# Optimization experiments

Measured on AMD Instinct MI355X. Metric: run time of the kernel, lower is better.

## Reference

```python
import jax, jax.numpy as jnp
import numpy as np


def setup_inputs() -> dict:
    key = jax.random.key(0)
    k1, k2 = jax.random.split(key)
    x = jax.random.normal(k1, (16, 1024, 512), dtype=jnp.float32)
    embedding = jax.random.normal(k2, (8192, 512), dtype=jnp.float32)
    return {"x": x, "embedding": embedding}


def reference(x, embedding):
    # x: [b, n, c], embedding (codebook k): [m, c]
    b, n, c = x.shape
    m = embedding.shape[0]
    q = x.reshape(b * n, c)            # (b n) c
    k = embedding
    # Squared L2 distance: ||q||^2 + ||k||^2 - 2 q.k  -> [bn, m]
    sim = (jnp.sum(q * q, axis=1, keepdims=True)
           + jnp.sum(k * k, axis=1)
           - 2.0 * jnp.einsum('nc,mc->nm', q, k))
    z_indices = jnp.argmin(sim, axis=1)                     # [bn]
    z_onehot = jax.nn.one_hot(z_indices, m, dtype=jnp.float32)  # [bn, m]
    # Direct gather is mathematically identical to onehot @ k
    z = k[z_indices]                                        # [bn, c]
    # Straight-through estimator: z = q + sg(z - q)
    z_st = q + jax.lax.stop_gradient(z - q)
    # Perplexity of code usage
    z_mean = jnp.mean(z_onehot, axis=0)                     # [m]
    perplexity = jnp.exp(-jnp.sum(z_mean * jnp.log(z_mean + 1e-10)))
    return (z_st.reshape(b, n, c),
            z_indices.reshape(b, n),
            z_onehot.reshape(b, n, m),
            perplexity)
```

## Files before the change

kernel.cpp:

```cpp
#include <hip/hip_runtime.h>
#include <cstdint>
#include <cstddef>

#define BNR 16384
#define C   512
#define M   8192
#define BM  128
#define BN  128
#define BK  64
#define NCH 8
#define NSETS 64

#define GEMM_BLOCKS 8192
#define NZ1 256
#define R1  8192
#define NZ2 128
#define R2  10240
#define FIN_FULL 1536
#define FIN_SCAT 40

#define TILE_U16   8192
#define PANEL_U16  65536

typedef float f32x4 __attribute__((ext_vector_type(4)));
typedef _Float16 f16x8 __attribute__((ext_vector_type(8)));
typedef unsigned short u16;

static __device__ __forceinline__ u16 h_bits(_Float16 h) {
    union { _Float16 h; u16 u; } x; x.h = h; return x.u;
}
static __device__ __forceinline__ void gl_lds16(const void* g, void* l) {
    __builtin_amdgcn_global_load_lds(
        (const __attribute__((address_space(1))) void*)g,
        (__attribute__((address_space(3))) void*)l, 16, 0, 0);
}

static __device__ __forceinline__ void cvt_unit(const float* __restrict__ in,
                                                u16* __restrict__ outp, int o) {
    int q = o & 1023, kb = q >> 7, row = q & 127;
    int c = (o >> 10) & 7, pan = o >> 13;
    int grow = pan * BM + row;
    int k0 = c * BK + kb * 8;
    const float4* src = (const float4*)(in + (size_t)grow * C + k0);
    float4 a = src[0], b = src[1];
    u16 v[8] = { h_bits((_Float16)a.x), h_bits((_Float16)a.y),
                 h_bits((_Float16)a.z), h_bits((_Float16)a.w),
                 h_bits((_Float16)b.x), h_bits((_Float16)b.y),
                 h_bits((_Float16)b.z), h_bits((_Float16)b.w) };
    u16* dst = outp + (size_t)o * 8;
    *(ushort4*)(dst)     = *(ushort4*)(v);
    *(ushort4*)(dst + 4) = *(ushort4*)(v + 4);
}

__global__ void prelude_k(const float* __restrict__ x, const float* __restrict__ emb,
                          u16* __restrict__ x2t, u16* __restrict__ e2t,
                          float* __restrict__ knorm) {
    int b = blockIdx.x;
    if (b < 4096) { cvt_unit(x, x2t, b * 256 + threadIdx.x); return; }
    if (b < 6144) { cvt_unit(emb, e2t, (b - 4096) * 256 + threadIdx.x); return; }
    int t = (b - 6144) * 256 + threadIdx.x;
    int gw = t >> 6, lane = t & 63;
    for (int row = gw; row < M; row += 256) {
        const float4* p = (const float4*)(emb + (size_t)row * C);
        float s = 0.f;
#pragma unroll
        for (int j = 0; j < 2; ++j) {
            float4 v = p[lane + 64 * j];
            s += v.x * v.x + v.y * v.y + v.z * v.z + v.w * v.w;
        }
#pragma unroll
        for (int o = 32; o > 0; o >>= 1) s += __shfl_down(s, o, 64);
        if (lane == 0) knorm[row] = s;
    }
}

__global__ void mega_k(
    const u16* __restrict__ x2t, const u16* __restrict__ e2t,
    const float* __restrict__ knorm,
    float* __restrict__ pv1, int* __restrict__ pi1,
    float* __restrict__ pv2, int* __restrict__ pi2,
    float* __restrict__ onehot) {
    __shared__ __align__(16) u16 ldsA[8][128][8];
    __shared__ __align__(16) u16 ldsB[8][128][8];

    if (blockIdx.x < NZ1) {
        f32x4* o4 = (f32x4*)onehot;
        size_t base = (size_t)blockIdx.x * 65536 + threadIdx.x;
        const f32x4 z = (f32x4)(0.0f);
#pragma unroll 4
        for (int i = 0; i < 256; ++i)
            __builtin_nontemporal_store(z, &o4[base + (size_t)i * 256]);
        return;
    }

    const int gid  = blockIdx.x - NZ1;
    const int tid  = threadIdx.x;
    const int lane = tid & 63;
    const int w    = tid >> 6;
    const int wm   = w >> 1, wn = w & 1;
    const int g    = lane >> 4, r = lane & 15;

    const int xk = gid & 7, j = gid >> 3;
    const int stid = (j >> 6) * 8 + xk;
    const int p  = j & 63;
    const int rb = (stid & 15) * 8 + (p & 7);
    const int cb = (stid >> 4) * 8 + (p >> 3);
    const int rowBase = rb * BM, colBase = cb * BN;

    f32x4 acc[4][4];
#pragma unroll
    for (int m = 0; m < 4; ++m)
#pragma unroll
        for (int n = 0; n < 4; ++n) acc[m][n] = (f32x4)(0.0f);

    const u16* aT = x2t + (size_t)rb * PANEL_U16;
    const u16* bT = e2t + (size_t)cb * PANEL_U16;

#pragma unroll 1
    for (int c = 0; c < NCH; ++c) {
        if (c) __syncthreads();
#pragma unroll
        for (int it = 0; it < 4; ++it) {
            int u = it * 256 + tid;
            gl_lds16(aT + (size_t)c * TILE_U16 + u * 8, (u16*)ldsA + u * 8);
            gl_lds16(bT + (size_t)c * TILE_U16 + u * 8, (u16*)ldsB + u * 8);
        }
        __syncthreads();

#pragma unroll
        for (int ks = 0; ks < 2; ++ks) {
            const int kb = ks * 4 + g;
            f16x8 a[4], b[4];
#pragma unroll
            for (int m = 0; m < 4; ++m)
                a[m] = *(const f16x8*)&ldsA[kb][wm * 64 + m * 16 + r][0];
#pragma unroll
            for (int n = 0; n < 4; ++n)
                b[n] = *(const f16x8*)&ldsB[kb][wn * 64 + n * 16 + r][0];
#pragma unroll
            for (int m = 0; m < 4; ++m)
#pragma unroll
                for (int n = 0; n < 4; ++n)
                    acc[m][n] = __builtin_amdgcn_mfma_f32_16x16x32_f16(
                        a[m], b[n], acc[m][n], 0, 0, 0);
        }
    }
    __syncthreads();

    float kn[4];
#pragma unroll
    for (int n = 0; n < 4; ++n) kn[n] = knorm[colBase + wn * 64 + n * 16 + r];

    float* mv = (float*)&ldsA[0][0][0];
    int*   mi = (int*)(mv + 2 * 128 * 2);

#pragma unroll
    for (int m = 0; m < 4; ++m) {
#pragma unroll
        for (int q = 0; q < 4; ++q) {
            float v1 = 3.0e38f, v2 = 3.0e38f;
            int   i1 = 0x7fffffff, i2 = 0x7fffffff;
#pragma unroll
            for (int n = 0; n < 4; ++n) {
                int col = colBase + wn * 64 + n * 16 + r;
                float d = fmaf(-2.0f, acc[m][n][q], kn[n]);
                if (d < v1 || (d == v1 && col < i1)) {
                    v2 = v1; i2 = i1; v1 = d; i1 = col;
                } else if (d < v2 || (d == v2 && col < i2)) {
                    v2 = d; i2 = col;
                }
            }
#pragma unroll
            for (int msk = 1; msk < 16; msk <<= 1) {
                float ov1 = __shfl_xor(v1, msk, 64);
                int   oi1 = __shfl_xor(i1, msk, 64);
                float ov2 = __shfl_xor(v2, msk, 64);
                int   oi2 = __shfl_xor(i2, msk, 64);
                bool ob = (ov1 < v1) || (ov1 == v1 && oi1 < i1);
                float nbv = ob ? ov1 : v1;  int nbi = ob ? oi1 : i1;
                float c1v = ob ? ov2 : v2;  int c1i = ob ? oi2 : i2;
                float c2v = ob ? v1 : ov1;  int c2i = ob ? i1 : oi1;
                bool cb2 = (c2v < c1v) || (c2v == c1v && c2i < c1i);
                v1 = nbv; i1 = nbi;
                v2 = cb2 ? c2v : c1v; i2 = cb2 ? c2i : c1i;
            }
            if (r == 0) {
                int lrow = wm * 64 + m * 16 + g * 4 + q;
                mv[(wn * 128 + lrow) * 2 + 0] = v1;
                mv[(wn * 128 + lrow) * 2 + 1] = v2;
                mi[(wn * 128 + lrow) * 2 + 0] = i1;
                mi[(wn * 128 + lrow) * 2 + 1] = i2;
            }
        }
    }
    __syncthreads();

    if (tid < 128) {
        float V1 = 3.0e38f, V2 = 3.0e38f;
        int   I1 = 0x7fffffff, I2 = 0x7fffffff;
#pragma unroll
        for (int s = 0; s < 4; ++s) {
            float d = mv[((s >> 1) * 128 + tid) * 2 + (s & 1)];
            int   ci = mi[((s >> 1) * 128 + tid) * 2 + (s & 1)];
            if (d < V1 || (d == V1 && ci < I1)) {
                V2 = V1; I2 = I1; V1 = d; I1 = ci;
            } else if (d < V2 || (d == V2 && ci < I2)) {
                V2 = d; I2 = ci;
            }
        }
        size_t o = (size_t)cb * BNR + rowBase + tid;
        pv1[o] = V1; pi1[o] = I1;
        pv2[o] = V2; pi2[o] = I2;
    }
}

__global__ void refine2_k(const float* __restrict__ x, const float* __restrict__ emb,
                          const float* __restrict__ pv1, const int* __restrict__ pi1,
                          const float* __restrict__ pv2, const int* __restrict__ pi2,
                          float* __restrict__ out_idx, float* __restrict__ zst,
                          float* __restrict__ onehot) {
    if (blockIdx.x < NZ2) {
        f32x4* o4 = (f32x4*)onehot;
        size_t base = (size_t)R1 * 2048 + (size_t)blockIdx.x * 32768 + threadIdx.x;
        const f32x4 z = (f32x4)(0.0f);
#pragma unroll 4
        for (int i = 0; i < 128; ++i)
            __builtin_nontemporal_store(z, &o4[base + (size_t)i * 256]);
        return;
    }
    int rid  = blockIdx.x - NZ2;
    int row  = rid * 4 + (threadIdx.x >> 6);
    int lane = threadIdx.x & 63;
    size_t off = (size_t)lane * BNR + row;
    float va = pv1[off]; int ia = pi1[off];
    float vb = pv2[off]; int ib = pi2[off];
    int cand[8];
#pragma unroll
    for (int b = 0; b < 8; ++b) {
        bool al = (va < vb) || (va == vb && ia < ib);
        float cv = al ? va : vb; int ci = al ? ia : ib;
#pragma unroll
        for (int msk = 1; msk < 64; msk <<= 1) {
            float ov = __shfl_xor(cv, msk, 64);
            int   oi = __shfl_xor(ci, msk, 64);
            if (ov < cv || (ov == cv && oi < ci)) { cv = ov; ci = oi; }
        }
        cand[b] = ci;
        if (ia == ci) va = 3.0e38f;
        else if (ib == ci) vb = 3.0e38f;
    }
    int gid = lane >> 3, gl = lane & 7;
    int myc = cand[gid];
    const float* qp = x + (size_t)row * C;
    const float* kp = emb + (size_t)myc * C;
    double s = 0.0;
#pragma unroll 4
    for (int j = gl * 64; j < gl * 64 + 64; j += 4) {
        float4 q4 = *(const float4*)(qp + j);
        float4 k4 = *(const float4*)(kp + j);
        double d0 = (double)q4.x - (double)k4.x;
        double d1 = (double)q4.y - (double)k4.y;
        double d2 = (double)q4.z - (double)k4.z;
        double d3 = (double)q4.w - (double)k4.w;
        s += d0 * d0 + d1 * d1 + d2 * d2 + d3 * d3;
    }
    s += __shfl_xor(s, 1, 64);
    s += __shfl_xor(s, 2, 64);
    s += __shfl_xor(s, 4, 64);
    double dv = s; int di = myc;
#pragma unroll
    for (int msk = 1; msk < 64; msk <<= 1) {
        double ov = __shfl_xor(dv, msk, 64);
        int    oi = __shfl_xor(di, msk, 64);
        if (ov < dv || (ov == dv && oi < di)) { dv = ov; di = oi; }
    }
    const f32x4* er = (const f32x4*)(emb + (size_t)di * C);
    f32x4* zr = (f32x4*)(zst + (size_t)row * C);
    __builtin_nontemporal_store(er[lane * 2],     &zr[lane * 2]);
    __builtin_nontemporal_store(er[lane * 2 + 1], &zr[lane * 2 + 1]);
    if (lane == 0) out_idx[row] = (float)di;
}

__global__ void finish_k(const float* __restrict__ out_idx,
                         float* __restrict__ onehot) {
    if (blockIdx.x < FIN_FULL) {
        int base = R2 + blockIdx.x * 4;
#pragma unroll
        for (int r4 = 0; r4 < 4; ++r4) {
            int row = base + r4;
            int idx = (int)out_idx[row];
            int hot4 = idx >> 2, hotc = idx & 3;
            f32x4* orow = (f32x4*)(onehot + (size_t)row * M);
#pragma unroll
            for (int t = 0; t < 8; ++t) {
                int j4 = t * 256 + threadIdx.x;
                f32x4 v = (f32x4)(0.0f);
                if (j4 == hot4) v[hotc] = 1.0f;
                __builtin_nontemporal_store(v, &orow[j4]);
            }
        }
        return;
    }
    int gid = (blockIdx.x - FIN_FULL) * 256 + threadIdx.x;
    if (gid < R2) {
        int idx = (int)out_idx[gid];
        onehot[(size_t)gid * M + idx] = 1.0f;
    }
}

__global__ void perp_k(const float* __restrict__ out_idx, float* __restrict__ out_perp) {
    __shared__ int hist[M];
    __shared__ float red[256];
    int tid = threadIdx.x;
    for (int j = tid; j < M; j += 256) hist[j] = 0;
    __syncthreads();
    for (int j = tid; j < BNR; j += 256) atomicAdd(&hist[(int)out_idx[j]], 1);
    __syncthreads();
    float s = 0.f;
    for (int j = tid; j < M; j += 256) {
        float pb = (float)hist[j] * (1.0f / (float)BNR);
        s += pb * logf(pb + 1e-10f);
    }
    red[tid] = s; __syncthreads();
    for (int o = 128; o > 0; o >>= 1) {
        if (tid < o) red[tid] += red[tid + o];
        __syncthreads();
    }
    if (tid == 0) out_perp[0] = expf(-red[0]);
}

extern "C" void kernel_launch(void* const* d_in, const int* in_sizes, int n_in,
                              void* d_out, int out_size, void* d_ws, size_t ws_size,
                              hipStream_t stream) {
    const float* x   = (const float*)d_in[0];
    const float* emb = (const float*)d_in[1];

    float* out        = (float*)d_out;
    float* out_zst    = out;
    float* out_idx    = out + (size_t)BNR * C;
    float* out_onehot = out_idx + BNR;
    float* out_perp   = out_onehot + (size_t)BNR * M;

    u16*   x2t   = (u16*)d_ws;
    u16*   e2t   = x2t + (size_t)BNR * C;
    float* knorm = (float*)(e2t + (size_t)M * C);
    float* pv1   = knorm + M;
    float* pv2   = pv1 + (size_t)NSETS * BNR;
    int*   pi1   = (int*)(pv2 + (size_t)NSETS * BNR);
    int*   pi2   = pi1 + (size_t)NSETS * BNR;

    prelude_k<<<6208, 256, 0, stream>>>(x, emb, x2t, e2t, knorm);
    mega_k<<<NZ1 + GEMM_BLOCKS, 256, 0, stream>>>(
        x2t, e2t, knorm, pv1, pi1, pv2, pi2, out_onehot);
    refine2_k<<<NZ2 + BNR / 4, 256, 0, stream>>>(
        x, emb, pv1, pi1, pv2, pi2, out_idx, out_zst, out_onehot);
    finish_k<<<FIN_FULL + FIN_SCAT, 256, 0, stream>>>(out_idx, out_onehot);
    perp_k<<<1, 256, 0, stream>>>(out_idx, out_perp);
}
```

Measured before the change: 452.1 us.

## Fuse one-hot writes into refine kernel and redistribute zero-fill across prelude and GEMM

Removes the separate finish kernel. The refine kernel now writes one-hot output directly: full rows for rows past R1 and a single scatter for earlier rows. Zero-filling of the first 8192 rows is moved so that 32 blocks run in the prelude and 224 blocks run alongside the GEMM, instead of 256 in the GEMM and 128 in refine. This saves a kernel launch and a reread of the indices, and spreads the output traffic to overlap with compute. The cost is that refine wavefronts with row >= R1 each write a full 32 KB row, which may lengthen the refine tail.

```diff
diff --git a/kernel.cpp b/kernel.cpp
--- a/kernel.cpp
+++ b/kernel.cpp
@@ -12,12 +12,10 @@
 #define NSETS 64
 
 #define GEMM_BLOCKS 8192
-#define NZ1 256
+#define NZP 32
+#define RZP 1024
+#define NZ1 224
 #define R1  8192
-#define NZ2 128
-#define R2  10240
-#define FIN_FULL 1536
-#define FIN_SCAT 40
 
 #define TILE_U16   8192
 #define PANEL_U16  65536
@@ -54,8 +52,18 @@
 
 __global__ void prelude_k(const float* __restrict__ x, const float* __restrict__ emb,
                           u16* __restrict__ x2t, u16* __restrict__ e2t,
-                          float* __restrict__ knorm) {
+                          float* __restrict__ knorm, float* __restrict__ onehot) {
     int b = blockIdx.x;
+    if (b < NZP) {
+        f32x4* o4 = (f32x4*)onehot;
+        size_t base = (size_t)b * 65536 + threadIdx.x;
+        const f32x4 z = (f32x4)(0.0f);
+#pragma unroll 4
+        for (int i = 0; i < 256; ++i)
+            __builtin_nontemporal_store(z, &o4[base + (size_t)i * 256]);
+        return;
+    }
+    b -= NZP;
     if (b < 4096) { cvt_unit(x, x2t, b * 256 + threadIdx.x); return; }
     if (b < 6144) { cvt_unit(emb, e2t, (b - 4096) * 256 + threadIdx.x); return; }
     int t = (b - 6144) * 256 + threadIdx.x;
@@ -85,7 +93,7 @@
 
     if (blockIdx.x < NZ1) {
         f32x4* o4 = (f32x4*)onehot;
-        size_t base = (size_t)blockIdx.x * 65536 + threadIdx.x;
+        size_t base = (size_t)RZP * 2048 + (size_t)blockIdx.x * 65536 + threadIdx.x;
         const f32x4 z = (f32x4)(0.0f);
 #pragma unroll 4
         for (int i = 0; i < 256; ++i)
@@ -214,22 +222,12 @@
     }
 }
 
-__global__ void refine2_k(const float* __restrict__ x, const float* __restrict__ emb,
+__global__ void refine3_k(const float* __restrict__ x, const float* __restrict__ emb,
                           const float* __restrict__ pv1, const int* __restrict__ pi1,
                           const float* __restrict__ pv2, const int* __restrict__ pi2,
                           float* __restrict__ out_idx, float* __restrict__ zst,
                           float* __restrict__ onehot) {
-    if (blockIdx.x < NZ2) {
-        f32x4* o4 = (f32x4*)onehot;
-        size_t base = (size_t)R1 * 2048 + (size_t)blockIdx.x * 32768 + threadIdx.x;
-        const f32x4 z = (f32x4)(0.0f);
-#pragma unroll 4
-        for (int i = 0; i < 128; ++i)
-            __builtin_nontemporal_store(z, &o4[base + (size_t)i * 256]);
-        return;
-    }
-    int rid  = blockIdx.x - NZ2;
-    int row  = rid * 4 + (threadIdx.x >> 6);
+    int row  = blockIdx.x * 4 + (threadIdx.x >> 6);
     int lane = threadIdx.x & 63;
     size_t off = (size_t)lane * BNR + row;
     float va = pv1[off]; int ia = pi1[off];
@@ -274,38 +272,26 @@
         int    oi = __shfl_xor(di, msk, 64);
         if (ov < dv || (ov == dv && oi < di)) { dv = ov; di = oi; }
     }
+
     const f32x4* er = (const f32x4*)(emb + (size_t)di * C);
     f32x4* zr = (f32x4*)(zst + (size_t)row * C);
     __builtin_nontemporal_store(er[lane * 2],     &zr[lane * 2]);
     __builtin_nontemporal_store(er[lane * 2 + 1], &zr[lane * 2 + 1]);
+
+    if (row >= R1) {
+        f32x4* orow = (f32x4*)(onehot + (size_t)row * M);
+        const int hot4 = di >> 2, hotc = di & 3;
+#pragma unroll
+        for (int i = 0; i < 32; ++i) {
+            int j4 = i * 64 + lane;
+            f32x4 v = (f32x4)(0.0f);
+            if (j4 == hot4) v[hotc] = 1.0f;
+            __builtin_nontemporal_store(v, &orow[j4]);
+        }
+    } else if (lane == 0) {
+        onehot[(size_t)row * M + di] = 1.0f;
+    }
     if (lane == 0) out_idx[row] = (float)di;
-}
-
-__global__ void finish_k(const float* __restrict__ out_idx,
-                         float* __restrict__ onehot) {
-    if (blockIdx.x < FIN_FULL) {
-        int base = R2 + blockIdx.x * 4;
-#pragma unroll
-        for (int r4 = 0; r4 < 4; ++r4) {
-            int row = base + r4;
-            int idx = (int)out_idx[row];
-            int hot4 = idx >> 2, hotc = idx & 3;
-            f32x4* orow = (f32x4*)(onehot + (size_t)row * M);
-#pragma unroll
-            for (int t = 0; t < 8; ++t) {
-                int j4 = t * 256 + threadIdx.x;
-                f32x4 v = (f32x4)(0.0f);
-                if (j4 == hot4) v[hotc] = 1.0f;
-                __builtin_nontemporal_store(v, &orow[j4]);
-            }
-        }
-        return;
-    }
-    int gid = (blockIdx.x - FIN_FULL) * 256 + threadIdx.x;
-    if (gid < R2) {
-        int idx = (int)out_idx[gid];
-        onehot[(size_t)gid * M + idx] = 1.0f;
-    }
 }
 
 __global__ void perp_k(const float* __restrict__ out_idx, float* __restrict__ out_perp) {
@@ -349,11 +335,10 @@
     int*   pi1   = (int*)(pv2 + (size_t)NSETS * BNR);
     int*   pi2   = pi1 + (size_t)NSETS * BNR;
 
-    prelude_k<<<6208, 256, 0, stream>>>(x, emb, x2t, e2t, knorm);
+    prelude_k<<<NZP + 6208, 256, 0, stream>>>(x, emb, x2t, e2t, knorm, out_onehot);
     mega_k<<<NZ1 + GEMM_BLOCKS, 256, 0, stream>>>(
         x2t, e2t, knorm, pv1, pi1, pv2, pi2, out_onehot);
-    refine2_k<<<NZ2 + BNR / 4, 256, 0, stream>>>(
+    refine3_k<<<BNR / 4, 256, 0, stream>>>(
         x, emb, pv1, pi1, pv2, pi2, out_idx, out_zst, out_onehot);
-    finish_k<<<FIN_FULL + FIN_SCAT, 256, 0, stream>>>(out_idx, out_onehot);
     perp_k<<<1, 256, 0, stream>>>(out_idx, out_perp);
 }
```

New measurement: 433.7 us. 1.04x faster.
